# Optimization experiments

Hardware: AMD Instinct MI355X
Metric: run time of the kernel (lower is better)

The kernel has to match this reference:

```python
import jax, jax.numpy as jnp
import numpy as np

MASK_OD = np.array([
    [False, False, False, True, True, True, True, False, False],
    [False, False, True, True, True, True, True, True, False],
    [False, True, True, True, True, True, True, True, True],
    [True, True, True, True, True, True, True, False, True],
    [True, True, True, True, True, True, True, False, True],
    [False, True, True, True, True, True, True, True, True],
    [False, False, True, True, True, True, True, True, False],
    [False, False, False, True, True, True, True, False, False]], dtype=bool)

SCALE = float(np.sqrt(128.0))  # sqrt(attn_dim)


def build_prior(num_points=52):
    # Faithful reproduction of _init_anatomical_prior (OD laterality, no flip)
    pr_grid = np.arange(196) // 14
    pc_grid = np.arange(196) % 14
    prior = np.zeros((num_points, 196), dtype=np.float32)
    vf_idx = 0
    for r in range(8):
        for c in range(9):
            if MASK_OD[r, c]:
                pr = 13 - int(r * 13 / 7)
                pc = 13 - int(c * 13 / 8)
                prior[vf_idx] = -((pr_grid - pr) ** 2 + (pc_grid - pc) ** 2) / (2.0 * 3.0 ** 2)
                vf_idx += 1
    return prior


def setup_inputs() -> dict:
    key = jax.random.key(0)
    ks = jax.random.split(key, 8)
    B, P, K, E, A = 256, 52, 196, 1024, 128
    return {
        "patches": jax.random.normal(ks[0], (B, K, E), jnp.float32),
        "queries": jax.random.normal(ks[1], (P, A), jnp.float32) * 0.02,
        "Wk": jax.random.normal(ks[2], (A, E), jnp.float32) / np.sqrt(E),
        "Wv": jax.random.normal(ks[3], (A, E), jnp.float32) / np.sqrt(E),
        "Wo": jax.random.normal(ks[4], (E, A), jnp.float32) / np.sqrt(A),
        "bo": jnp.zeros((E,), jnp.float32),
        "patch_pos": jax.random.normal(ks[5], (K, A), jnp.float32) * 0.02,
        "temperature": jnp.asarray(2.0, jnp.float32),
        "attn_prior": jnp.asarray(build_prior(P)),
    }


def reference(patches, queries, Wk, Wv, Wo, bo, patch_pos, temperature, attn_prior):
    # patches: [B, 196, E]; laterality fixed to 'OD' (no prior flip)
    keys = jnp.einsum('bke,ae->bka', patches, Wk) + patch_pos  # [B, 196, A]
    vals = jnp.einsum('bke,ae->bka', patches, Wv)              # [B, 196, A]
    logits = jnp.einsum('qa,bka->bqk', queries, keys) / SCALE  # [B, 52, 196]
    temp = jax.nn.softplus(temperature) + 0.5
    logits = (logits + attn_prior[None]) / temp
    attn_weights = jax.nn.softmax(logits, axis=-1)
    # dropout is identity in eval mode
    attended = jnp.einsum('bqk,bka->bqa', attn_weights, vals)  # [B, 52, A]
    out = jnp.einsum('bqa,ea->bqe', attended, Wo) + bo         # [B, 52, E]
    return out, attn_weights
```

## Files before the change

### kernel.cpp

```cpp
#include <hip/hip_runtime.h>

typedef __attribute__((ext_vector_type(8))) short bf16x8;
typedef __attribute__((ext_vector_type(4))) short bf16x4;
typedef __attribute__((ext_vector_type(4))) float f32x4;
typedef __attribute__((ext_vector_type(4))) float floatx4;

__device__ __forceinline__ unsigned short f2bf(float f) {
    unsigned int u = __float_as_uint(f);
    u += 0x7fffu + ((u >> 16) & 1u);
    return (unsigned short)(u >> 16);
}
__device__ __forceinline__ float bf2f_s(short h) {
    return __uint_as_float(((unsigned int)(unsigned short)h) << 16);
}

__device__ __forceinline__ void gload_lds16(const void* gsrc, void* ldst) {
    __builtin_amdgcn_global_load_lds(
        (const __attribute__((address_space(1))) unsigned int*)gsrc,
        (__attribute__((address_space(3))) unsigned int*)ldst, 16, 0, 0);
}

__device__ __forceinline__ bf16x8 cvt8(f32x4 lo, f32x4 hi) {
    union { unsigned int u[4]; bf16x8 v; } r;
    asm("v_cvt_pk_bf16_f32 %0, %1, %2" : "=v"(r.u[0]) : "v"(lo[0]), "v"(lo[1]));
    asm("v_cvt_pk_bf16_f32 %0, %1, %2" : "=v"(r.u[1]) : "v"(lo[2]), "v"(lo[3]));
    asm("v_cvt_pk_bf16_f32 %0, %1, %2" : "=v"(r.u[2]) : "v"(hi[0]), "v"(hi[1]));
    asm("v_cvt_pk_bf16_f32 %0, %1, %2" : "=v"(r.u[3]) : "v"(hi[2]), "v"(hi[3]));
    return r.v;
}

__global__ void k_convert(const float* __restrict__ Wk, const float* __restrict__ Wv,
                          const float* __restrict__ Wo,
                          unsigned short* __restrict__ Wkvb, unsigned short* __restrict__ Wob) {
    int i = (blockIdx.x * blockDim.x + threadIdx.x) * 4;
    if (i < 131072) {
        floatx4 a = *reinterpret_cast<const floatx4*>(Wk + i);
        floatx4 b = *reinterpret_cast<const floatx4*>(Wv + i);
        floatx4 c = *reinterpret_cast<const floatx4*>(Wo + i);
        bf16x4 sa, sb, sc;
        #pragma unroll
        for (int e = 0; e < 4; ++e) {
            sa[e] = (short)f2bf(a[e]); sb[e] = (short)f2bf(b[e]); sc[e] = (short)f2bf(c[e]);
        }
        *reinterpret_cast<bf16x4*>(Wkvb + i)          = sa;
        *reinterpret_cast<bf16x4*>(Wkvb + 131072 + i) = sb;
        *reinterpret_cast<bf16x4*>(Wob + i)           = sc;
    }
}

__global__ __launch_bounds__(256, 4)
void k_keysvals(const float* __restrict__ patches,
                const unsigned short* __restrict__ Wkvb,
                const float* __restrict__ patch_pos,
                unsigned short* __restrict__ kv)
{
    __shared__ float          As[64 * 64];
    __shared__ unsigned short Bs[128 * 64];

    const int tid  = threadIdx.x;
    const int lane = tid & 63;
    const int wave = tid >> 6;
    const int wm   = wave >> 1;
    const int wn   = wave & 1;
    const int l15  = lane & 15;
    const int lg   = lane >> 4;

    const int bid  = blockIdx.x;
    const int nb   = bid & 1;
    const int mt   = bid >> 1;
    const int row0 = mt * 64;
    const int n0   = nb * 128;

    const int arow = tid >> 4;
    const int agn  = (tid & 15) ^ arow;
    const char* agbase = (const char*)(patches + (size_t)(row0 + arow) * 1024) + agn * 16;

    const int brow = tid >> 3;
    const int bgn  = (tid & 7) ^ (brow & 7);
    const char* bgbase = (const char*)(Wkvb + (size_t)(n0 + brow) * 1024) + bgn * 16;

    char* alds = (char*)As + tid * 16;
    char* blds = (char*)Bs + tid * 16;

    f32x4 acc[2][4];
    #pragma unroll
    for (int i = 0; i < 2; ++i)
        #pragma unroll
        for (int j = 0; j < 4; ++j)
            acc[i][j] = (f32x4){0.f, 0.f, 0.f, 0.f};

    for (int t = 0; t < 16; ++t) {
        const int koA = t * 256;
        const int koB = t * 128;
        #pragma unroll
        for (int i = 0; i < 4; ++i)
            gload_lds16(agbase + (size_t)i * 65536 + koA, alds + i * 4096);
        #pragma unroll
        for (int i = 0; i < 4; ++i)
            gload_lds16(bgbase + (size_t)i * 65536 + koB, blds + i * 4096);
        __syncthreads();

        #pragma unroll
        for (int kk = 0; kk < 2; ++kk) {
            bf16x8 af[2];
            #pragma unroll
            for (int mi = 0; mi < 2; ++mi) {
                const int mrow = wm * 32 + mi * 16 + l15;
                const int q0   = (kk * 8 + lg * 2) ^ l15;
                const int q1   = q0 ^ 1;
                f32x4 lo = *reinterpret_cast<const f32x4*>((const char*)As + mrow * 256 + q0 * 16);
                f32x4 hi = *reinterpret_cast<const f32x4*>((const char*)As + mrow * 256 + q1 * 16);
                af[mi] = cvt8(lo, hi);
            }
            #pragma unroll
            for (int ni = 0; ni < 4; ++ni) {
                const int nrow = wn * 64 + ni * 16 + l15;
                const int qb   = (kk * 4 + lg) ^ (l15 & 7);
                bf16x8 bf = *reinterpret_cast<const bf16x8*>((const char*)Bs + nrow * 128 + qb * 16);
                #pragma unroll
                for (int mi = 0; mi < 2; ++mi)
                    acc[mi][ni] = __builtin_amdgcn_mfma_f32_16x16x32_bf16(af[mi], bf, acc[mi][ni], 0, 0, 0);
            }
        }
        __syncthreads();
    }

    #pragma unroll
    for (int mi = 0; mi < 2; ++mi) {
        #pragma unroll
        for (int i = 0; i < 4; ++i) {
            int m  = row0 + wm * 32 + mi * 16 + lg * 4 + i;
            int kp = m % 196;
            #pragma unroll
            for (int ni = 0; ni < 4; ++ni) {
                int n = n0 + wn * 64 + ni * 16 + l15;
                float v = acc[mi][ni][i];
                if (n < 128) v += patch_pos[kp * 128 + n];
                kv[(size_t)m * 256 + n] = f2bf(v);
            }
        }
    }
}

__global__ __launch_bounds__(1024)
void k_attn(const unsigned short* __restrict__ kv,
            const float* __restrict__ queries,
            const float* __restrict__ prior,
            const float* __restrict__ temperature,
            float* __restrict__ attn_out,
            unsigned short* __restrict__ att)
{
    __shared__ unsigned short k_s[196][136];
    __shared__ unsigned short v_s[196][128];
    __shared__ unsigned short q_s[52][128];
    __shared__ float          l_s[52][196];

    const int b   = blockIdx.x;
    const int tid = threadIdx.x;
    const size_t base = (size_t)b * 196 * 256;

    for (int idx = tid; idx < 6272; idx += 1024) {
        int row = idx >> 5;
        int c   = (idx & 31) * 8;
        bf16x8 v = *reinterpret_cast<const bf16x8*>(kv + base + row * 256 + c);
        if (c < 128) *reinterpret_cast<bf16x8*>(&k_s[row][c])       = v;
        else         *reinterpret_cast<bf16x8*>(&v_s[row][c - 128]) = v;
    }
    for (int idx = tid; idx < 1664; idx += 1024) {
        int row = idx >> 5;
        int c   = (idx & 31) * 4;
        const float* qp = queries + row * 128 + c;
        bf16x4 sv;
        sv[0] = (short)f2bf(qp[0]); sv[1] = (short)f2bf(qp[1]);
        sv[2] = (short)f2bf(qp[2]); sv[3] = (short)f2bf(qp[3]);
        *reinterpret_cast<bf16x4*>(&q_s[row][c]) = sv;
    }
    __syncthreads();

    const float inv_temp  = 1.0f / (log1pf(expf(temperature[0])) + 0.5f);
    const float inv_scale = 0.08838834764831845f;

    for (int task = tid; task < 3328; task += 1024) {
        int q  = task >> 6;
        int kg = task & 63;
        if (kg < 49) {
            float dot0 = 0.f, dot1 = 0.f, dot2 = 0.f, dot3 = 0.f;
            #pragma unroll 4
            for (int c = 0; c < 128; c += 8) {
                bf16x8 qv = *reinterpret_cast<const bf16x8*>(&q_s[q][c]);
                float qf[8];
                #pragma unroll
                for (int e = 0; e < 8; ++e) qf[e] = bf2f_s(qv[e]);
                bf16x8 k0v = *reinterpret_cast<const bf16x8*>(&k_s[kg][c]);
                bf16x8 k1v = *reinterpret_cast<const bf16x8*>(&k_s[kg + 49][c]);
                bf16x8 k2v = *reinterpret_cast<const bf16x8*>(&k_s[kg + 98][c]);
                bf16x8 k3v = *reinterpret_cast<const bf16x8*>(&k_s[kg + 147][c]);
                #pragma unroll
                for (int e = 0; e < 8; ++e) {
                    dot0 += qf[e] * bf2f_s(k0v[e]);
                    dot1 += qf[e] * bf2f_s(k1v[e]);
                    dot2 += qf[e] * bf2f_s(k2v[e]);
                    dot3 += qf[e] * bf2f_s(k3v[e]);
                }
            }
            int k;
            k = kg;       l_s[q][k] = (dot0 * inv_scale + prior[q * 196 + k]) * inv_temp;
            k = kg + 49;  l_s[q][k] = (dot1 * inv_scale + prior[q * 196 + k]) * inv_temp;
            k = kg + 98;  l_s[q][k] = (dot2 * inv_scale + prior[q * 196 + k]) * inv_temp;
            k = kg + 147; l_s[q][k] = (dot3 * inv_scale + prior[q * 196 + k]) * inv_temp;
        }
    }
    __syncthreads();

    const int lane = tid & 63;
    const int wave = tid >> 6;
    for (int q = wave; q < 52; q += 16) {
        float x0 = l_s[q][lane];
        float x1 = l_s[q][lane + 64];
        float x2 = l_s[q][lane + 128];
        float x3 = (lane < 4) ? l_s[q][lane + 192] : -1e30f;
        float m = fmaxf(fmaxf(x0, x1), fmaxf(x2, x3));
        #pragma unroll
        for (int off = 32; off > 0; off >>= 1) m = fmaxf(m, __shfl_xor(m, off));
        float e0 = expf(x0 - m), e1 = expf(x1 - m), e2 = expf(x2 - m);
        float e3 = (lane < 4) ? expf(x3 - m) : 0.0f;
        float s = e0 + e1 + e2 + e3;
        #pragma unroll
        for (int off = 32; off > 0; off >>= 1) s += __shfl_xor(s, off);
        float inv = 1.0f / s;
        float* po = attn_out + ((size_t)b * 52 + q) * 196;
        float a0 = e0 * inv, a1 = e1 * inv, a2 = e2 * inv;
        l_s[q][lane]       = a0;  po[lane]       = a0;
        l_s[q][lane + 64]  = a1;  po[lane + 64]  = a1;
        l_s[q][lane + 128] = a2;  po[lane + 128] = a2;
        if (lane < 4) { float a3 = e3 * inv; l_s[q][lane + 192] = a3; po[lane + 192] = a3; }
    }
    __syncthreads();

    if (tid < 832) {
        int q  = tid >> 4;
        int a0 = (tid & 15) * 8;
        float accv[8] = {0.f, 0.f, 0.f, 0.f, 0.f, 0.f, 0.f, 0.f};
        for (int k = 0; k < 196; ++k) {
            float w = l_s[q][k];
            bf16x8 vv = *reinterpret_cast<const bf16x8*>(&v_s[k][a0]);
            #pragma unroll
            for (int e = 0; e < 8; ++e) accv[e] += w * bf2f_s(vv[e]);
        }
        bf16x8 sv;
        #pragma unroll
        for (int e = 0; e < 8; ++e) sv[e] = (short)f2bf(accv[e]);
        *reinterpret_cast<bf16x8*>(att + ((size_t)b * 52 + q) * 128 + a0) = sv;
    }
}

__global__ __launch_bounds__(512)
void k_out(const unsigned short* __restrict__ att,
           const unsigned short* __restrict__ Wob,
           const float* __restrict__ bo,
           float* __restrict__ out)
{
    __shared__ unsigned short As[64][72];
    __shared__ unsigned short Bs[256][72];

    const int tid  = threadIdx.x;
    const int lane = tid & 63;
    const int wave = tid >> 6;
    const int wm   = wave >> 2;
    const int wn   = wave & 3;
    const int l15  = lane & 15;
    const int lg   = lane >> 4;
    const int row0 = blockIdx.x * 64;
    const int e0   = blockIdx.y * 256;

    f32x4 acc[2][4];
    #pragma unroll
    for (int i = 0; i < 2; ++i)
        #pragma unroll
        for (int j = 0; j < 4; ++j)
            acc[i][j] = (f32x4){0.f, 0.f, 0.f, 0.f};

    for (int ko = 0; ko < 128; ko += 64) {
        {
            int r = tid >> 3;
            int c = (tid & 7) * 8;
            bf16x8 v = *reinterpret_cast<const bf16x8*>(att + (size_t)(row0 + r) * 128 + ko + c);
            *reinterpret_cast<bf16x8*>(&As[r][c]) = v;
        }
        {
            int r = tid >> 3;
            int c = (tid & 7) * 8;
            #pragma unroll
            for (int it = 0; it < 4; ++it) {
                bf16x8 v = *reinterpret_cast<const bf16x8*>(Wob + (size_t)(e0 + it * 64 + r) * 128 + ko + c);
                *reinterpret_cast<bf16x8*>(&Bs[it * 64 + r][c]) = v;
            }
        }
        __syncthreads();
        #pragma unroll
        for (int kk = 0; kk < 2; ++kk) {
            bf16x8 af[2], bfr[4];
            #pragma unroll
            for (int mi = 0; mi < 2; ++mi)
                af[mi] = *reinterpret_cast<const bf16x8*>(&As[wm * 32 + mi * 16 + l15][kk * 32 + lg * 8]);
            #pragma unroll
            for (int ni = 0; ni < 4; ++ni)
                bfr[ni] = *reinterpret_cast<const bf16x8*>(&Bs[wn * 64 + ni * 16 + l15][kk * 32 + lg * 8]);
            #pragma unroll
            for (int mi = 0; mi < 2; ++mi)
                #pragma unroll
                for (int ni = 0; ni < 4; ++ni)
                    acc[mi][ni] = __builtin_amdgcn_mfma_f32_16x16x32_bf16(af[mi], bfr[ni], acc[mi][ni], 0, 0, 0);
        }
        __syncthreads();
    }
    #pragma unroll
    for (int mi = 0; mi < 2; ++mi) {
        #pragma unroll
        for (int i = 0; i < 4; ++i) {
            int m = row0 + wm * 32 + mi * 16 + lg * 4 + i;
            #pragma unroll
            for (int ni = 0; ni < 4; ++ni) {
                int e = e0 + wn * 64 + ni * 16 + l15;
                out[(size_t)m * 1024 + e] = acc[mi][ni][i] + bo[e];
            }
        }
    }
}

extern "C" void kernel_launch(void* const* d_in, const int* in_sizes, int n_in,
                              void* d_out, int out_size, void* d_ws, size_t ws_size,
                              hipStream_t stream)
{
    const float* patches     = (const float*)d_in[0];
    const float* queries     = (const float*)d_in[1];
    const float* Wk          = (const float*)d_in[2];
    const float* Wv          = (const float*)d_in[3];
    const float* Wo          = (const float*)d_in[4];
    const float* bo          = (const float*)d_in[5];
    const float* patch_pos   = (const float*)d_in[6];
    const float* temperature = (const float*)d_in[7];
    const float* prior       = (const float*)d_in[8];

    float* out      = (float*)d_out;
    float* attn_out = out + (size_t)256 * 52 * 1024;

    unsigned short* Wkvb = (unsigned short*)d_ws;
    unsigned short* Wob  = Wkvb + 256 * 1024;
    unsigned short* kv   = Wob + 1024 * 128;
    unsigned short* att  = kv + (size_t)50176 * 256;

    k_convert <<<128, 256, 0, stream>>>(Wk, Wv, Wo, Wkvb, Wob);
    k_keysvals<<<1568, 256, 0, stream>>>(patches, Wkvb, patch_pos, kv);
    k_attn    <<<256, 1024, 0, stream>>>(kv, queries, prior, temperature, attn_out, att);
    k_out     <<<dim3(208, 4), 512, 0, stream>>>(att, Wob, bo, out);
}
```

Before: 158.9 us.

## Double-buffer LDS tiles in keys/values GEMM to overlap loads with MFMA

Doubles the shared-memory A and B tiles so the next K-slice is issued via global_load_lds while the current slice is consumed by MFMAs, leaving one barrier per iteration instead of two. It also lowers launch bounds occupancy from 4 to 2 blocks per CU to fit the doubled LDS (~64KB per block). The aim is to hide global load latency, at the cost of fewer resident waves to hide latency by switching.

```diff
diff --git a/kernel.cpp b/kernel.cpp
--- a/kernel.cpp
+++ b/kernel.cpp
@@ -48,14 +48,14 @@
     }
 }
 
-__global__ __launch_bounds__(256, 4)
+__global__ __launch_bounds__(256, 2)
 void k_keysvals(const float* __restrict__ patches,
                 const unsigned short* __restrict__ Wkvb,
                 const float* __restrict__ patch_pos,
                 unsigned short* __restrict__ kv)
 {
-    __shared__ float          As[64 * 64];
-    __shared__ unsigned short Bs[128 * 64];
+    __shared__ float          As[2][64 * 64];
+    __shared__ unsigned short Bs[2][128 * 64];
 
     const int tid  = threadIdx.x;
     const int lane = tid & 63;
@@ -79,9 +79,6 @@
     const int bgn  = (tid & 7) ^ (brow & 7);
     const char* bgbase = (const char*)(Wkvb + (size_t)(n0 + brow) * 1024) + bgn * 16;
 
-    char* alds = (char*)As + tid * 16;
-    char* blds = (char*)Bs + tid * 16;
-
     f32x4 acc[2][4];
     #pragma unroll
     for (int i = 0; i < 2; ++i)
@@ -89,16 +86,32 @@
         for (int j = 0; j < 4; ++j)
             acc[i][j] = (f32x4){0.f, 0.f, 0.f, 0.f};
 
+    {
+        char* al = (char*)As[0] + tid * 16;
+        char* bl = (char*)Bs[0] + tid * 16;
+        #pragma unroll
+        for (int i = 0; i < 4; ++i)
+            gload_lds16(agbase + (size_t)i * 65536, al + i * 4096);
+        #pragma unroll
+        for (int i = 0; i < 4; ++i)
+            gload_lds16(bgbase + (size_t)i * 65536, bl + i * 4096);
+    }
+    __syncthreads();
+
+    int cur = 0;
     for (int t = 0; t < 16; ++t) {
-        const int koA = t * 256;
-        const int koB = t * 128;
-        #pragma unroll
-        for (int i = 0; i < 4; ++i)
-            gload_lds16(agbase + (size_t)i * 65536 + koA, alds + i * 4096);
-        #pragma unroll
-        for (int i = 0; i < 4; ++i)
-            gload_lds16(bgbase + (size_t)i * 65536 + koB, blds + i * 4096);
-        __syncthreads();
+        if (t < 15) {
+            const int koA = (t + 1) * 256;
+            const int koB = (t + 1) * 128;
+            char* al = (char*)As[cur ^ 1] + tid * 16;
+            char* bl = (char*)Bs[cur ^ 1] + tid * 16;
+            #pragma unroll
+            for (int i = 0; i < 4; ++i)
+                gload_lds16(agbase + (size_t)i * 65536 + koA, al + i * 4096);
+            #pragma unroll
+            for (int i = 0; i < 4; ++i)
+                gload_lds16(bgbase + (size_t)i * 65536 + koB, bl + i * 4096);
+        }
 
         #pragma unroll
         for (int kk = 0; kk < 2; ++kk) {
@@ -108,21 +121,25 @@
                 const int mrow = wm * 32 + mi * 16 + l15;
                 const int q0   = (kk * 8 + lg * 2) ^ l15;
                 const int q1   = q0 ^ 1;
-                f32x4 lo = *reinterpret_cast<const f32x4*>((const char*)As + mrow * 256 + q0 * 16);
-                f32x4 hi = *reinterpret_cast<const f32x4*>((const char*)As + mrow * 256 + q1 * 16);
+                f32x4 lo = *reinterpret_cast<const f32x4*>((const char*)As[cur] + mrow * 256 + q0 * 16);
+                f32x4 hi = *reinterpret_cast<const f32x4*>((const char*)As[cur] + mrow * 256 + q1 * 16);
                 af[mi] = cvt8(lo, hi);
             }
             #pragma unroll
             for (int ni = 0; ni < 4; ++ni) {
                 const int nrow = wn * 64 + ni * 16 + l15;
                 const int qb   = (kk * 4 + lg) ^ (l15 & 7);
-                bf16x8 bf = *reinterpret_cast<const bf16x8*>((const char*)Bs + nrow * 128 + qb * 16);
+                bf16x8 bf = *reinterpret_cast<const bf16x8*>((const char*)Bs[cur] + nrow * 128 + qb * 16);
                 #pragma unroll
                 for (int mi = 0; mi < 2; ++mi)
                     acc[mi][ni] = __builtin_amdgcn_mfma_f32_16x16x32_bf16(af[mi], bf, acc[mi][ni], 0, 0, 0);
             }
         }
-        __syncthreads();
+
+        if (t < 15) {
+            __syncthreads();
+            cur ^= 1;
+        }
     }
 
     #pragma unroll
```

Result: slower. 176.2 us (+10.8%).

## Triple-buffer keys/values GEMM and merge N-halves into one 512-thread block

Applied to the files above, without the earlier changes.

The keys/values projection kernel now gives each block a 64x256 output tile (both K and V halves) with 8 waves, so each block loads the patch rows once instead of twice. The K loop uses a three-stage LDS ring with global_load_lds prefetch and explicit vmcnt waits, so loads for later stages overlap MFMA work on the current one. This costs 144KB of LDS per block and fewer concurrently resident blocks, and the hand-written waitcnt counts have to match the number of issued loads exactly.

```diff
diff --git a/kernel.cpp b/kernel.cpp
--- a/kernel.cpp
+++ b/kernel.cpp
@@ -48,39 +48,31 @@
     }
 }
 
-__global__ __launch_bounds__(256, 4)
+__global__ __launch_bounds__(512, 2)
 void k_keysvals(const float* __restrict__ patches,
                 const unsigned short* __restrict__ Wkvb,
                 const float* __restrict__ patch_pos,
                 unsigned short* __restrict__ kv)
 {
-    __shared__ float          As[64 * 64];
-    __shared__ unsigned short Bs[128 * 64];
+    __shared__ char lds[3][49152];
 
     const int tid  = threadIdx.x;
     const int lane = tid & 63;
     const int wave = tid >> 6;
-    const int wm   = wave >> 1;
-    const int wn   = wave & 1;
+    const int wm   = wave >> 2;
+    const int wn   = wave & 3;
     const int l15  = lane & 15;
     const int lg   = lane >> 4;
-
-    const int bid  = blockIdx.x;
-    const int nb   = bid & 1;
-    const int mt   = bid >> 1;
-    const int row0 = mt * 64;
-    const int n0   = nb * 128;
+    const int row0 = blockIdx.x * 64;
 
     const int arow = tid >> 4;
-    const int agn  = (tid & 15) ^ arow;
-    const char* agbase = (const char*)(patches + (size_t)(row0 + arow) * 1024) + agn * 16;
+    const int aga  = (tid & 15) ^ (arow & 15);
+    const char* ag0 = (const char*)(patches + (size_t)(row0 + arow) * 1024) + aga * 16;
+    const char* ag1 = (const char*)(patches + (size_t)(row0 + arow + 32) * 1024) + aga * 16;
 
     const int brow = tid >> 3;
-    const int bgn  = (tid & 7) ^ (brow & 7);
-    const char* bgbase = (const char*)(Wkvb + (size_t)(n0 + brow) * 1024) + bgn * 16;
-
-    char* alds = (char*)As + tid * 16;
-    char* blds = (char*)Bs + tid * 16;
+    const int bg   = (tid & 7) ^ (brow & 7);
+    const char* bg0 = (const char*)(Wkvb + (size_t)brow * 1024) + bg * 16;
 
     f32x4 acc[2][4];
     #pragma unroll
@@ -89,17 +81,20 @@
         for (int j = 0; j < 4; ++j)
             acc[i][j] = (f32x4){0.f, 0.f, 0.f, 0.f};
 
-    for (int t = 0; t < 16; ++t) {
-        const int koA = t * 256;
-        const int koB = t * 128;
-        #pragma unroll
-        for (int i = 0; i < 4; ++i)
-            gload_lds16(agbase + (size_t)i * 65536 + koA, alds + i * 4096);
-        #pragma unroll
-        for (int i = 0; i < 4; ++i)
-            gload_lds16(bgbase + (size_t)i * 65536 + koB, blds + i * 4096);
-        __syncthreads();
-
+    auto stage = [&](int s) {
+        char* dst = lds[s % 3] + tid * 16;
+        const int koA = s * 256;
+        const int koB = s * 128;
+        gload_lds16(ag0 + koA, dst);
+        gload_lds16(ag1 + koA, dst + 8192);
+        #pragma unroll
+        for (int it = 0; it < 4; ++it)
+            gload_lds16(bg0 + (size_t)it * 131072 + koB, dst + 16384 + it * 8192);
+    };
+
+    auto compute = [&](const char* buf) {
+        const char* As = buf;
+        const char* Bs = buf + 16384;
         #pragma unroll
         for (int kk = 0; kk < 2; ++kk) {
             bf16x8 af[2];
@@ -108,21 +103,39 @@
                 const int mrow = wm * 32 + mi * 16 + l15;
                 const int q0   = (kk * 8 + lg * 2) ^ l15;
                 const int q1   = q0 ^ 1;
-                f32x4 lo = *reinterpret_cast<const f32x4*>((const char*)As + mrow * 256 + q0 * 16);
-                f32x4 hi = *reinterpret_cast<const f32x4*>((const char*)As + mrow * 256 + q1 * 16);
+                f32x4 lo = *reinterpret_cast<const f32x4*>(As + mrow * 256 + q0 * 16);
+                f32x4 hi = *reinterpret_cast<const f32x4*>(As + mrow * 256 + q1 * 16);
                 af[mi] = cvt8(lo, hi);
             }
             #pragma unroll
             for (int ni = 0; ni < 4; ++ni) {
                 const int nrow = wn * 64 + ni * 16 + l15;
                 const int qb   = (kk * 4 + lg) ^ (l15 & 7);
-                bf16x8 bf = *reinterpret_cast<const bf16x8*>((const char*)Bs + nrow * 128 + qb * 16);
+                bf16x8 bf = *reinterpret_cast<const bf16x8*>(Bs + nrow * 128 + qb * 16);
                 #pragma unroll
                 for (int mi = 0; mi < 2; ++mi)
                     acc[mi][ni] = __builtin_amdgcn_mfma_f32_16x16x32_bf16(af[mi], bf, acc[mi][ni], 0, 0, 0);
             }
         }
-        __syncthreads();
+    };
+
+    stage(0); stage(1); stage(2);
+
+    #pragma unroll
+    for (int t = 0; t < 16; ++t) {
+        if (t < 14)       asm volatile("s_waitcnt vmcnt(12)" ::: "memory");
+        else if (t == 14) asm volatile("s_waitcnt vmcnt(6)" ::: "memory");
+        else              asm volatile("s_waitcnt vmcnt(0)" ::: "memory");
+        __builtin_amdgcn_s_barrier();
+        __builtin_amdgcn_sched_barrier(0);
+
+        compute(lds[t % 3]);
+
+        if (t < 13) {
+            __builtin_amdgcn_sched_barrier(0);
+            __builtin_amdgcn_s_barrier();
+            stage(t + 3);
+        }
     }
 
     #pragma unroll
@@ -133,7 +146,7 @@
             int kp = m % 196;
             #pragma unroll
             for (int ni = 0; ni < 4; ++ni) {
-                int n = n0 + wn * 64 + ni * 16 + l15;
+                int n = wn * 64 + ni * 16 + l15;
                 float v = acc[mi][ni][i];
                 if (n < 128) v += patch_pos[kp * 128 + n];
                 kv[(size_t)m * 256 + n] = f2bf(v);
@@ -351,7 +364,7 @@
     unsigned short* att  = kv + (size_t)50176 * 256;
 
     k_convert <<<128, 256, 0, stream>>>(Wk, Wv, Wo, Wkvb, Wob);
-    k_keysvals<<<1568, 256, 0, stream>>>(patches, Wkvb, patch_pos, kv);
+    k_keysvals<<<784, 512, 0, stream>>>(patches, Wkvb, patch_pos, kv);
     k_attn    <<<256, 1024, 0, stream>>>(kv, queries, prior, temperature, attn_out, att);
     k_out     <<<dim3(208, 4), 512, 0, stream>>>(att, Wob, bo, out);
 }
```

After: 167.4 us. +5.4%, slower.

## Restructure keys/values GEMM to one batch per block with register-staged double buffering

Applied to the files above, without the earlier changes.

Each block now computes the full 196x256 key/value tile for one batch, so the fp32 patches are read from global memory once instead of once per column half. A tiles are loaded into registers, converted to bf16, and written to a padded, double-buffered LDS while the previous tile is being multiplied. The weight conversion kernel also uses packed bf16 conversion instructions. The cost is a grid of only 256 large blocks, high register use for accumulators, and a 208-row padded tile that wastes some MFMA work.

```diff
diff --git a/kernel.cpp b/kernel.cpp
--- a/kernel.cpp
+++ b/kernel.cpp
@@ -12,12 +12,6 @@
 }
 __device__ __forceinline__ float bf2f_s(short h) {
     return __uint_as_float(((unsigned int)(unsigned short)h) << 16);
-}
-
-__device__ __forceinline__ void gload_lds16(const void* gsrc, void* ldst) {
-    __builtin_amdgcn_global_load_lds(
-        (const __attribute__((address_space(1))) unsigned int*)gsrc,
-        (__attribute__((address_space(3))) unsigned int*)ldst, 16, 0, 0);
 }
 
 __device__ __forceinline__ bf16x8 cvt8(f32x4 lo, f32x4 hi) {
@@ -27,6 +21,12 @@
     asm("v_cvt_pk_bf16_f32 %0, %1, %2" : "=v"(r.u[2]) : "v"(hi[0]), "v"(hi[1]));
     asm("v_cvt_pk_bf16_f32 %0, %1, %2" : "=v"(r.u[3]) : "v"(hi[2]), "v"(hi[3]));
     return r.v;
+}
+__device__ __forceinline__ bf16x4 cvt4(f32x4 v) {
+    union { unsigned int u[2]; bf16x4 x; } r;
+    asm("v_cvt_pk_bf16_f32 %0, %1, %2" : "=v"(r.u[0]) : "v"(v[0]), "v"(v[1]));
+    asm("v_cvt_pk_bf16_f32 %0, %1, %2" : "=v"(r.u[1]) : "v"(v[2]), "v"(v[3]));
+    return r.x;
 }
 
 __global__ void k_convert(const float* __restrict__ Wk, const float* __restrict__ Wv,
@@ -37,106 +37,116 @@
         floatx4 a = *reinterpret_cast<const floatx4*>(Wk + i);
         floatx4 b = *reinterpret_cast<const floatx4*>(Wv + i);
         floatx4 c = *reinterpret_cast<const floatx4*>(Wo + i);
-        bf16x4 sa, sb, sc;
-        #pragma unroll
-        for (int e = 0; e < 4; ++e) {
-            sa[e] = (short)f2bf(a[e]); sb[e] = (short)f2bf(b[e]); sc[e] = (short)f2bf(c[e]);
-        }
-        *reinterpret_cast<bf16x4*>(Wkvb + i)          = sa;
-        *reinterpret_cast<bf16x4*>(Wkvb + 131072 + i) = sb;
-        *reinterpret_cast<bf16x4*>(Wob + i)           = sc;
-    }
-}
-
-__global__ __launch_bounds__(256, 4)
+        *reinterpret_cast<bf16x4*>(Wkvb + i)          = cvt4(a);
+        *reinterpret_cast<bf16x4*>(Wkvb + 131072 + i) = cvt4(b);
+        *reinterpret_cast<bf16x4*>(Wob + i)           = cvt4(c);
+    }
+}
+
+__global__ __launch_bounds__(512)
 void k_keysvals(const float* __restrict__ patches,
                 const unsigned short* __restrict__ Wkvb,
                 const float* __restrict__ patch_pos,
                 unsigned short* __restrict__ kv)
 {
-    __shared__ float          As[64 * 64];
-    __shared__ unsigned short Bs[128 * 64];
+    __shared__ unsigned short As[2][208][72];
+    __shared__ unsigned short Bs[2][256][72];
 
     const int tid  = threadIdx.x;
     const int lane = tid & 63;
-    const int wave = tid >> 6;
-    const int wm   = wave >> 1;
-    const int wn   = wave & 1;
+    const int w    = tid >> 6;
     const int l15  = lane & 15;
     const int lg   = lane >> 4;
-
-    const int bid  = blockIdx.x;
-    const int nb   = bid & 1;
-    const int mt   = bid >> 1;
-    const int row0 = mt * 64;
-    const int n0   = nb * 128;
-
-    const int arow = tid >> 4;
-    const int agn  = (tid & 15) ^ arow;
-    const char* agbase = (const char*)(patches + (size_t)(row0 + arow) * 1024) + agn * 16;
-
-    const int brow = tid >> 3;
-    const int bgn  = (tid & 7) ^ (brow & 7);
-    const char* bgbase = (const char*)(Wkvb + (size_t)(n0 + brow) * 1024) + bgn * 16;
-
-    char* alds = (char*)As + tid * 16;
-    char* blds = (char*)Bs + tid * 16;
-
-    f32x4 acc[2][4];
+    const int b    = blockIdx.x;
+    const float* abase = patches + (size_t)b * 196 * 1024;
+
+    const int brow = tid >> 1;
+    const int bh   = tid & 1;
+    const unsigned short* bgp = Wkvb + (size_t)brow * 1024 + bh * 32;
+
+    f32x4  aH[7];
+    bf16x8 bH[4];
+
+    f32x4 acc[13][2];
     #pragma unroll
-    for (int i = 0; i < 2; ++i)
+    for (int i = 0; i < 13; ++i) {
+        acc[i][0] = (f32x4){0.f, 0.f, 0.f, 0.f};
+        acc[i][1] = (f32x4){0.f, 0.f, 0.f, 0.f};
+    }
+
+    auto issue = [&](int t) {
+        const int ko = t * 64;
+        #pragma unroll
+        for (int i = 0; i < 6; ++i) {
+            int g = tid + i * 512;
+            int r = g >> 4, gc = g & 15;
+            aH[i] = *reinterpret_cast<const f32x4*>(abase + (size_t)r * 1024 + ko + gc * 4);
+        }
+        if (tid < 64) {
+            int g = 3072 + tid;
+            int r = g >> 4, gc = g & 15;
+            aH[6] = *reinterpret_cast<const f32x4*>(abase + (size_t)r * 1024 + ko + gc * 4);
+        }
         #pragma unroll
         for (int j = 0; j < 4; ++j)
-            acc[i][j] = (f32x4){0.f, 0.f, 0.f, 0.f};
+            bH[j] = *reinterpret_cast<const bf16x8*>(bgp + ko + j * 8);
+    };
+    auto store = [&](int buf) {
+        #pragma unroll
+        for (int i = 0; i < 6; ++i) {
+            int g = tid + i * 512;
+            int r = g >> 4, gc = g & 15;
+            *reinterpret_cast<bf16x4*>(&As[buf][r][gc * 4]) = cvt4(aH[i]);
+        }
+        if (tid < 64) {
+            int g = 3072 + tid;
+            int r = g >> 4, gc = g & 15;
+            *reinterpret_cast<bf16x4*>(&As[buf][r][gc * 4]) = cvt4(aH[6]);
+        }
+        #pragma unroll
+        for (int j = 0; j < 4; ++j)
+            *reinterpret_cast<bf16x8*>(&Bs[buf][brow][bh * 32 + j * 8]) = bH[j];
+    };
+    auto compute = [&](int buf) {
+        #pragma unroll
+        for (int kk = 0; kk < 2; ++kk) {
+            bf16x8 bf[2];
+            #pragma unroll
+            for (int nf = 0; nf < 2; ++nf)
+                bf[nf] = *reinterpret_cast<const bf16x8*>(&Bs[buf][w * 32 + nf * 16 + l15][kk * 32 + lg * 8]);
+            #pragma unroll
+            for (int mf = 0; mf < 13; ++mf) {
+                bf16x8 af = *reinterpret_cast<const bf16x8*>(&As[buf][mf * 16 + l15][kk * 32 + lg * 8]);
+                acc[mf][0] = __builtin_amdgcn_mfma_f32_16x16x32_bf16(af, bf[0], acc[mf][0], 0, 0, 0);
+                acc[mf][1] = __builtin_amdgcn_mfma_f32_16x16x32_bf16(af, bf[1], acc[mf][1], 0, 0, 0);
+            }
+        }
+    };
+
+    issue(0);
+    store(0);
+    __syncthreads();
 
     for (int t = 0; t < 16; ++t) {
-        const int koA = t * 256;
-        const int koB = t * 128;
-        #pragma unroll
-        for (int i = 0; i < 4; ++i)
-            gload_lds16(agbase + (size_t)i * 65536 + koA, alds + i * 4096);
-        #pragma unroll
-        for (int i = 0; i < 4; ++i)
-            gload_lds16(bgbase + (size_t)i * 65536 + koB, blds + i * 4096);
+        if (t < 15) issue(t + 1);
+        compute(t & 1);
+        if (t < 15) store((t + 1) & 1);
         __syncthreads();
-
-        #pragma unroll
-        for (int kk = 0; kk < 2; ++kk) {
-            bf16x8 af[2];
-            #pragma unroll
-            for (int mi = 0; mi < 2; ++mi) {
-                const int mrow = wm * 32 + mi * 16 + l15;
-                const int q0   = (kk * 8 + lg * 2) ^ l15;
-                const int q1   = q0 ^ 1;
-                f32x4 lo = *reinterpret_cast<const f32x4*>((const char*)As + mrow * 256 + q0 * 16);
-                f32x4 hi = *reinterpret_cast<const f32x4*>((const char*)As + mrow * 256 + q1 * 16);
-                af[mi] = cvt8(lo, hi);
-            }
-            #pragma unroll
-            for (int ni = 0; ni < 4; ++ni) {
-                const int nrow = wn * 64 + ni * 16 + l15;
-                const int qb   = (kk * 4 + lg) ^ (l15 & 7);
-                bf16x8 bf = *reinterpret_cast<const bf16x8*>((const char*)Bs + nrow * 128 + qb * 16);
+    }
+
+    #pragma unroll
+    for (int mf = 0; mf < 13; ++mf) {
+        #pragma unroll
+        for (int i = 0; i < 4; ++i) {
+            int ml = mf * 16 + lg * 4 + i;
+            if (ml < 196) {
                 #pragma unroll
-                for (int mi = 0; mi < 2; ++mi)
-                    acc[mi][ni] = __builtin_amdgcn_mfma_f32_16x16x32_bf16(af[mi], bf, acc[mi][ni], 0, 0, 0);
-            }
-        }
-        __syncthreads();
-    }
-
-    #pragma unroll
-    for (int mi = 0; mi < 2; ++mi) {
-        #pragma unroll
-        for (int i = 0; i < 4; ++i) {
-            int m  = row0 + wm * 32 + mi * 16 + lg * 4 + i;
-            int kp = m % 196;
-            #pragma unroll
-            for (int ni = 0; ni < 4; ++ni) {
-                int n = n0 + wn * 64 + ni * 16 + l15;
-                float v = acc[mi][ni][i];
-                if (n < 128) v += patch_pos[kp * 128 + n];
-                kv[(size_t)m * 256 + n] = f2bf(v);
+                for (int nf = 0; nf < 2; ++nf) {
+                    int n = w * 32 + nf * 16 + l15;
+                    float v = acc[mf][nf][i];
+                    if (n < 128) v += patch_pos[ml * 128 + n];
+                    kv[((size_t)b * 196 + ml) * 256 + n] = f2bf(v);
+                }
             }
         }
     }
@@ -242,10 +252,10 @@
         int a0 = (tid & 15) * 8;
         float accv[8] = {0.f, 0.f, 0.f, 0.f, 0.f, 0.f, 0.f, 0.f};
         for (int k = 0; k < 196; ++k) {
-            float w = l_s[q][k];
+            float wgt = l_s[q][k];
             bf16x8 vv = *reinterpret_cast<const bf16x8*>(&v_s[k][a0]);
             #pragma unroll
-            for (int e = 0; e < 8; ++e) accv[e] += w * bf2f_s(vv[e]);
+            for (int e = 0; e < 8; ++e) accv[e] += wgt * bf2f_s(vv[e]);
         }
         bf16x8 sv;
         #pragma unroll
@@ -351,7 +361,7 @@
     unsigned short* att  = kv + (size_t)50176 * 256;
 
     k_convert <<<128, 256, 0, stream>>>(Wk, Wv, Wo, Wkvb, Wob);
-    k_keysvals<<<1568, 256, 0, stream>>>(patches, Wkvb, patch_pos, kv);
+    k_keysvals<<<256, 512, 0, stream>>>(patches, Wkvb, patch_pos, kv);
     k_attn    <<<256, 1024, 0, stream>>>(kv, queries, prior, temperature, attn_out, att);
     k_out     <<<dim3(208, 4), 512, 0, stream>>>(att, Wob, bo, out);
 }
```

Result: faster. 145.8 us (-8.3%).
